# Kernel tuning notes

Hardware: AMD Instinct MI355X
Metric: run time of the kernel (lower is better)

Reference implementation:

```python
import jax, jax.numpy as jnp
import numpy as np

B, N, E = 4, 2048, 16384
ND, ED, TD, C, H = 256, 128, 64, 512, 8
DH = C // H
EPS = 1e-5


def setup_inputs() -> dict:
    key = jax.random.key(0)
    ks = jax.random.split(key, 28)
    w = lambda k, s: (jax.random.normal(k, s, jnp.float32) * 0.02)
    inp = {
        'x': jax.random.normal(ks[0], (B, N, ND), jnp.float32),
        'edge_attr': jax.random.normal(ks[1], (B, E, ED), jnp.float32),
        'timestamps': jax.random.uniform(ks[2], (B, N), jnp.float32),
        # FeatureProjection / TimeEncoder params (torch Linear layout: [out,in])
        'W_node': w(ks[3], (C, 2 * ND)), 'b_node': jnp.zeros((C,), jnp.float32),
        'W_temb': w(ks[4], (TD, 1)),     'b_temb': jnp.zeros((TD,), jnp.float32),
        'W_timef': w(ks[5], (C, 2 * TD)), 'b_timef': jnp.zeros((C,), jnp.float32),
        'W_edge': w(ks[6], (C, ED)),     'b_edge': jnp.zeros((C,), jnp.float32),
        # MultiheadAttention params
        'Wq': w(ks[7], (C, C)), 'bq': jnp.zeros((C,), jnp.float32),
        'Wk': w(ks[8], (C, C)), 'bk': jnp.zeros((C,), jnp.float32),
        'Wv': w(ks[9], (C, C)), 'bv': jnp.zeros((C,), jnp.float32),
        'Wo': w(ks[10], (C, C)), 'bo': jnp.zeros((C,), jnp.float32),
        # FFN
        'W1': w(ks[11], (4 * C, C)), 'b1': jnp.zeros((4 * C,), jnp.float32),
        'W2': w(ks[12], (C, 4 * C)), 'b2': jnp.zeros((C,), jnp.float32),
        # LayerNorms
        'g1': jnp.ones((C,), jnp.float32), 'be1': jnp.zeros((C,), jnp.float32),
        'g2': jnp.ones((C,), jnp.float32), 'be2': jnp.zeros((C,), jnp.float32),
        'edge_index': jax.random.randint(ks[13], (B, 2, E), 0, N, jnp.int64),
    }
    return inp


def _ln(x, g, b):
    m = jnp.mean(x, axis=-1, keepdims=True)
    v = jnp.mean((x - m) ** 2, axis=-1, keepdims=True)
    return (x - m) * jax.lax.rsqrt(v + EPS) * g + b


def reference(x, edge_attr, timestamps, W_node, b_node, W_temb, b_temb,
              W_timef, b_timef, W_edge, b_edge, Wq, bq, Wk, bk, Wv, bv,
              Wo, bo, W1, b1, W2, b2, g1, be1, g2, be2, edge_index):
    Bx, Nx, _ = x.shape
    # add self-loops
    loops = jnp.broadcast_to(jnp.arange(Nx, dtype=edge_index.dtype)[None, None, :], (Bx, 2, Nx))
    ei = jnp.concatenate([edge_index, loops], axis=2)          # [B,2,E+N]
    ea = jnp.concatenate([edge_attr, jnp.zeros((Bx, Nx, edge_attr.shape[-1]), edge_attr.dtype)], axis=1)
    src, tgt = ei[:, 0, :], ei[:, 1, :]                        # [B,Et]
    # batched gathers
    x_i = jnp.take_along_axis(x, src[:, :, None], axis=1)      # [B,Et,ND]
    x_j = jnp.take_along_axis(x, tgt[:, :, None], axis=1)
    t_i = jnp.take_along_axis(timestamps, src, axis=1)         # [B,Et]
    t_j = jnp.take_along_axis(timestamps, tgt, axis=1)
    # time encoder: sin(Linear(1->TD))
    t_i_enc = jnp.sin(t_i[..., None] * W_temb[:, 0] + b_temb)  # [B,Et,TD]
    t_j_enc = jnp.sin(t_j[..., None] * W_temb[:, 0] + b_temb)
    # projections (torch Linear: y = x @ W.T + b)
    node_f = jnp.concatenate([x_i, x_j], axis=-1) @ W_node.T + b_node        # [B,Et,C]
    time_f = jnp.concatenate([t_i_enc, t_j_enc], axis=-1) @ W_timef.T + b_timef
    edge_f = ea @ W_edge.T + b_edge
    # MultiheadAttention, batch_first=False: seq axis = dim0 (length B)
    L, Nb, _ = node_f.shape
    q = (node_f @ Wq.T + bq).reshape(L, Nb, H, DH)
    k = (time_f @ Wk.T + bk).reshape(L, Nb, H, DH)
    v = (edge_f @ Wv.T + bv).reshape(L, Nb, H, DH)
    scores = jnp.einsum('lnhd,mnhd->nhlm', q, k) / np.sqrt(DH)  # [Nb,H,L,L]
    attn = jax.nn.softmax(scores, axis=-1)
    ctx = jnp.einsum('nhlm,mnhd->lnhd', attn, v).reshape(L, Nb, C)
    attn_out = ctx @ Wo.T + bo
    out1 = _ln(node_f + attn_out, g1, be1)
    ffn = jax.nn.gelu(out1 @ W1.T + b1, approximate=False) @ W2.T + b2
    out2 = _ln(out1 + ffn, g2, be2)
    return out2
```

## Files before the change

### kernel.cpp

```cpp
#include <hip/hip_runtime.h>
#include <math.h>

#define BB 4
#define NN 2048
#define EE 16384
#define LL (EE + NN)
#define ND_ 256
#define ED_ 128
#define TD_ 64
#define CC 512
#define HH 8
#define DH_ 64
#define C4 2048

typedef unsigned short u16;
typedef unsigned int u32;
typedef __bf16 bhalf8 __attribute__((ext_vector_type(8)));
typedef float f32x4 __attribute__((ext_vector_type(4)));

struct GatherArgs {
    const float* x;
    const float* ts;
    const float* wtemb;
    const float* btemb;
    const float* eattr;
    const int*   ei;
};

__device__ __forceinline__ u16 f2bf(float f) {
    union { float f; unsigned u; } c; c.f = f;
    const unsigned r = (c.u + 0x7fffu + ((c.u >> 16) & 1u)) >> 16;
    return (u16)r;
}
__device__ __forceinline__ u16 f2bf_hw(float f) {
    __bf16 h = (__bf16)f;
    union { __bf16 h; u16 u; } c; c.h = h; return c.u;
}
__device__ __forceinline__ float bf2f(u16 u) {
    union { unsigned u; float f; } c; c.u = ((unsigned)u) << 16; return c.f;
}
__device__ __forceinline__ float gelu_fast(float v) {
    const float u = v * (0.7978845608f + 0.0356774081f * v * v);
    const float e = __expf(2.0f * u);
    const float t = 1.0f - 2.0f / (e + 1.0f);
    return 0.5f * v * (1.0f + t);
}

#define GLD16(gp, lp) __builtin_amdgcn_global_load_lds( \
    (const __attribute__((address_space(1))) unsigned int*)(gp), \
    (__attribute__((address_space(3))) unsigned int*)(lp), 16, 0, 0)

template<bool GELU>
__global__ __launch_bounds__(512, 2)
void gemm_mfma(const u16* __restrict__ A, const u16* __restrict__ W,
               const float* __restrict__ bias, u16* __restrict__ Y,
               int N, int K)
{
    __shared__ u16 As[2][16384];
    __shared__ u16 Bs[2][16384];

    const int o    = blockIdx.y * gridDim.x + blockIdx.x;
    const int nwg  = gridDim.x * gridDim.y;
    const int xcd  = o & 7;
    const int qq   = nwg >> 3, rr = nwg & 7;
    const int wg   = (xcd < rr ? xcd * (qq + 1) : rr * (qq + 1) + (xcd - rr) * qq) + (o >> 3);
    const int bx   = wg % gridDim.x;
    const int by   = wg / gridDim.x;
    const int m0   = by * 256;
    const int n0   = bx * 256;

    const int tid  = threadIdx.x;
    const int lane = tid & 63;
    const int wid  = tid >> 6;
    const int wm   = wid >> 2;
    const int wn   = wid & 3;

    const int swz8 = (((tid & 7) ^ ((tid >> 3) & 7))) * 8;
    const size_t sK = (size_t)K;
    const u16* Agb = A + (size_t)(m0 + (tid >> 3)) * sK + swz8;
    const u16* Wgb = W + (size_t)(n0 + (tid >> 3)) * sK + swz8;

    const int NT  = K >> 6;
    const int rlo = lane & 15;
    const int hi4 = lane >> 4;
    const int lk  = lane & 7;

#define STAGE_A(kt, h) do {                                      \
    const u16* _g = Agb + (size_t)(kt) * 64 + (size_t)(h) * 128 * sK; \
    u16* _l = &As[(kt) & 1][(h) * 8192 + tid * 8];               \
    GLD16(_g,           _l);                                     \
    GLD16(_g + 64 * sK, _l + 4096);                              \
} while (0)
#define STAGE_B(kt, h) do {                                      \
    const u16* _g = Wgb + (size_t)(kt) * 64 + (size_t)(h) * 128 * sK; \
    u16* _l = &Bs[(kt) & 1][(h) * 8192 + tid * 8];               \
    GLD16(_g,           _l);                                     \
    GLD16(_g + 64 * sK, _l + 4096);                              \
} while (0)

#define SWZOFF(ks) (((((ks) << 2) | hi4) ^ lk) << 3)
#define RD(buf, row, ks) (*(const bhalf8*)&(buf)[(row) * 64 + SWZOFF(ks)])

#define PHASE_SYNC() do {                                        \
    __builtin_amdgcn_sched_barrier(0);                           \
    __builtin_amdgcn_s_barrier();                                \
    asm volatile("s_waitcnt lgkmcnt(0)" ::: "memory");           \
    __builtin_amdgcn_sched_barrier(0);                           \
} while (0)
#define PHASE_END() do {                                         \
    __builtin_amdgcn_sched_barrier(0);                           \
    __builtin_amdgcn_s_barrier();                                \
    __builtin_amdgcn_sched_barrier(0);                           \
} while (0)

    f32x4 acc[8][4] = {};

    STAGE_A(0, 0); STAGE_A(0, 1);
    STAGE_B(0, 0); STAGE_B(0, 1);
    STAGE_B(1, 0); STAGE_B(1, 1);
    asm volatile("s_waitcnt vmcnt(4)" ::: "memory");
    __builtin_amdgcn_s_barrier();
    __builtin_amdgcn_sched_barrier(0);

    for (int t = 0; t < NT; ++t) {
        const u16* as = &As[t & 1][0];
        const u16* bs = &Bs[t & 1][0];
        bhalf8 aLo[4][2], aHi[4][2], b0[2][2], b1[2][2];

        #pragma unroll
        for (int i = 0; i < 4; ++i) {
            aLo[i][0] = RD(as, wm * 128 + i * 16 + rlo, 0);
            aLo[i][1] = RD(as, wm * 128 + i * 16 + rlo, 1);
        }
        #pragma unroll
        for (int j = 0; j < 2; ++j) {
            b0[j][0] = RD(bs, wn * 64 + j * 16 + rlo, 0);
            b0[j][1] = RD(bs, wn * 64 + j * 16 + rlo, 1);
        }
        if (t + 1 < NT) STAGE_A(t + 1, 0);
        PHASE_SYNC();
        __builtin_amdgcn_s_setprio(1);
        #pragma unroll
        for (int i = 0; i < 4; ++i)
            #pragma unroll
            for (int j = 0; j < 2; ++j)
                #pragma unroll
                for (int ks = 0; ks < 2; ++ks)
                    acc[i][j] = __builtin_amdgcn_mfma_f32_16x16x32_bf16(b0[j][ks], aLo[i][ks], acc[i][j], 0, 0, 0);
        __builtin_amdgcn_s_setprio(0);
        PHASE_END();

        #pragma unroll
        for (int j = 0; j < 2; ++j) {
            b1[j][0] = RD(bs, wn * 64 + 32 + j * 16 + rlo, 0);
            b1[j][1] = RD(bs, wn * 64 + 32 + j * 16 + rlo, 1);
        }
        if (t + 1 < NT) STAGE_A(t + 1, 1);
        PHASE_SYNC();
        __builtin_amdgcn_s_setprio(1);
        #pragma unroll
        for (int i = 0; i < 4; ++i)
            #pragma unroll
            for (int j = 0; j < 2; ++j)
                #pragma unroll
                for (int ks = 0; ks < 2; ++ks)
                    acc[i][2 + j] = __builtin_amdgcn_mfma_f32_16x16x32_bf16(b1[j][ks], aLo[i][ks], acc[i][2 + j], 0, 0, 0);
        __builtin_amdgcn_s_setprio(0);
        PHASE_END();

        #pragma unroll
        for (int i = 0; i < 4; ++i) {
            aHi[i][0] = RD(as, wm * 128 + 64 + i * 16 + rlo, 0);
            aHi[i][1] = RD(as, wm * 128 + 64 + i * 16 + rlo, 1);
        }
        if (t + 2 < NT) STAGE_B(t + 2, 0);
        PHASE_SYNC();
        __builtin_amdgcn_s_setprio(1);
        #pragma unroll
        for (int i = 0; i < 4; ++i)
            #pragma unroll
            for (int j = 0; j < 2; ++j)
                #pragma unroll
                for (int ks = 0; ks < 2; ++ks)
                    acc[4 + i][j] = __builtin_amdgcn_mfma_f32_16x16x32_bf16(b0[j][ks], aHi[i][ks], acc[4 + i][j], 0, 0, 0);
        __builtin_amdgcn_s_setprio(0);
        PHASE_END();

        if (t + 2 < NT) {
            STAGE_B(t + 2, 1);
            asm volatile("s_waitcnt vmcnt(4)" ::: "memory");
        } else if (t < NT - 1) {
            asm volatile("s_waitcnt vmcnt(0)" ::: "memory");
        }
        PHASE_SYNC();
        __builtin_amdgcn_s_setprio(1);
        #pragma unroll
        for (int i = 0; i < 4; ++i)
            #pragma unroll
            for (int j = 0; j < 2; ++j)
                #pragma unroll
                for (int ks = 0; ks < 2; ++ks)
                    acc[4 + i][2 + j] = __builtin_amdgcn_mfma_f32_16x16x32_bf16(b1[j][ks], aHi[i][ks], acc[4 + i][2 + j], 0, 0, 0);
        __builtin_amdgcn_s_setprio(0);
        if (t < NT - 1) PHASE_END();
    }
#undef STAGE_A
#undef STAGE_B
#undef SWZOFF
#undef RD
#undef PHASE_SYNC
#undef PHASE_END

    const int row0 = m0 + wm * 128;
    const int col0 = n0 + wn * 64;
    const int rq   = (lane >> 4) * 4;
    float4 bi[4];
    #pragma unroll
    for (int j = 0; j < 4; ++j)
        bi[j] = *(const float4*)(bias + col0 + j * 16 + rq);

    #pragma unroll
    for (int i = 0; i < 8; ++i) {
        const int gr = row0 + i * 16 + rlo;
        u16* yrow = Y + (size_t)gr * N + col0;
        #pragma unroll
        for (int j = 0; j < 4; ++j) {
            float v0 = acc[i][j][0] + bi[j].x;
            float v1 = acc[i][j][1] + bi[j].y;
            float v2 = acc[i][j][2] + bi[j].z;
            float v3 = acc[i][j][3] + bi[j].w;
            if constexpr (GELU) {
                v0 = gelu_fast(v0); v1 = gelu_fast(v1);
                v2 = gelu_fast(v2); v3 = gelu_fast(v3);
            }
            ushort4 ov;
            ov.x = f2bf_hw(v0); ov.y = f2bf_hw(v1);
            ov.z = f2bf_hw(v2); ov.w = f2bf_hw(v3);
            *(ushort4*)(yrow + j * 16 + rq) = ov;
        }
    }
}

__global__ __launch_bounds__(256)
void prep_kernel(u16* __restrict__ An, u16* __restrict__ Akv,
                 int e0, GatherArgs ga)
{
    const int r  = blockIdx.x;
    const int el = r >> 2;
    const int b  = r & 3;
    const int ge = e0 + el;
    const int t  = threadIdx.x;

    int isrc, itgt;
    if (ge < EE) {
        isrc = ga.ei[(b * 2 + 0) * EE + ge];
        itgt = ga.ei[(b * 2 + 1) * EE + ge];
    } else {
        isrc = itgt = ge - EE;
    }

    if (t < 128) {
        const int c = t * 4;
        const float* src = (c < ND_) ? (ga.x + ((size_t)b * NN + isrc) * ND_ + c)
                                     : (ga.x + ((size_t)b * NN + itgt) * ND_ + (c - ND_));
        const float4 vv = *(const float4*)src;
        ushort4 ov;
        ov.x = f2bf(vv.x); ov.y = f2bf(vv.y); ov.z = f2bf(vv.z); ov.w = f2bf(vv.w);
        *(ushort4*)(An + (size_t)r * 512 + c) = ov;
    } else if (t < 160) {
        const int c  = (t - 128) * 4;
        const float tt = (c < TD_) ? ga.ts[b * NN + isrc] : ga.ts[b * NN + itgt];
        const int  cb = (c < TD_) ? c : c - TD_;
        ushort4 ov;
        ov.x = f2bf(sinf(tt * ga.wtemb[cb + 0] + ga.btemb[cb + 0]));
        ov.y = f2bf(sinf(tt * ga.wtemb[cb + 1] + ga.btemb[cb + 1]));
        ov.z = f2bf(sinf(tt * ga.wtemb[cb + 2] + ga.btemb[cb + 2]));
        ov.w = f2bf(sinf(tt * ga.wtemb[cb + 3] + ga.btemb[cb + 3]));
        *(ushort4*)(Akv + (size_t)r * 256 + c) = ov;
    } else if (t < 192) {
        const int c = (t - 160) * 4;
        float4 vv = make_float4(0.f, 0.f, 0.f, 0.f);
        if (ge < EE) vv = *(const float4*)(ga.eattr + ((size_t)b * EE + ge) * ED_ + c);
        ushort4 ov;
        ov.x = f2bf(vv.x); ov.y = f2bf(vv.y); ov.z = f2bf(vv.z); ov.w = f2bf(vv.w);
        *(ushort4*)(Akv + (size_t)r * 256 + 128 + c) = ov;
    }
}

__global__ __launch_bounds__(256)
void comb_w_bf(const float* __restrict__ Wa, const float* __restrict__ Wb,
               u16* __restrict__ out, int Kin, int ostride)
{
    const int idx  = blockIdx.x * 256 + threadIdx.x;
    const int c    = idx / Kin;
    const int kcol = idx - c * Kin;
    float acc = 0.f;
    for (int j = 0; j < CC; j++)
        acc += Wa[c * CC + j] * Wb[j * Kin + kcol];
    out[(size_t)c * ostride + kcol] = f2bf(acc);
}

__global__ __launch_bounds__(256)
void comb_b(const float* __restrict__ Wa, const float* __restrict__ bin,
            const float* __restrict__ ba, float* __restrict__ bout)
{
    const int c = blockIdx.x * 256 + threadIdx.x;
    float acc = ba[c];
    for (int j = 0; j < CC; j++)
        acc += Wa[c * CC + j] * bin[j];
    bout[c] = acc;
}

__global__ __launch_bounds__(256)
void cvt_bf(const float* __restrict__ in, u16* __restrict__ out, int n)
{
    const int i = (blockIdx.x * 256 + threadIdx.x) * 4;
    if (i < n) {
        const float4 v = *(const float4*)(in + i);
        ushort4 ov;
        ov.x = f2bf(v.x); ov.y = f2bf(v.y); ov.z = f2bf(v.z); ov.w = f2bf(v.w);
        *(ushort4*)(out + i) = ov;
    }
}

__global__ __launch_bounds__(256)
void zero_u16(u16* __restrict__ p, int n)
{
    const int i = blockIdx.x * 256 + threadIdx.x;
    if (i < n) p[i] = 0;
}

__global__ __launch_bounds__(256)
void copy_f32(const float* __restrict__ in, float* __restrict__ out, int n)
{
    const int i = blockIdx.x * 256 + threadIdx.x;
    if (i < n) out[i] = in[i];
}

__global__ __launch_bounds__(256)
void attn_kernel(const u16* __restrict__ nodq, const u16* __restrict__ kv,
                 u16* __restrict__ ctx)
{
    const int e    = blockIdx.x * 4 + (threadIdx.x >> 6);
    const int lane = threadIdx.x & 63;
    const int off  = (lane >> 3) * 64 + (lane & 7) * 8;

    float qf[4][8], kf[4][8], vf[4][8];
    #pragma unroll
    for (int l = 0; l < 4; l++) {
        const size_t rq = (size_t)(4 * e + l) * 1024;
        const uint4 qv = *(const uint4*)(nodq + rq + 512 + off);
        const uint4 kx = *(const uint4*)(kv + rq + off);
        const uint4 vx = *(const uint4*)(kv + rq + 512 + off);
        const u32 qa[4] = {qv.x, qv.y, qv.z, qv.w};
        const u32 ka[4] = {kx.x, kx.y, kx.z, kx.w};
        const u32 va[4] = {vx.x, vx.y, vx.z, vx.w};
        #pragma unroll
        for (int p = 0; p < 4; p++) {
            qf[l][2*p] = bf2f((u16)qa[p]); qf[l][2*p+1] = bf2f((u16)(qa[p] >> 16));
            kf[l][2*p] = bf2f((u16)ka[p]); kf[l][2*p+1] = bf2f((u16)(ka[p] >> 16));
            vf[l][2*p] = bf2f((u16)va[p]); vf[l][2*p+1] = bf2f((u16)(va[p] >> 16));
        }
    }

    float sc[4][4];
    #pragma unroll
    for (int l = 0; l < 4; l++) {
        #pragma unroll
        for (int m = 0; m < 4; m++) {
            float p = 0.f;
            #pragma unroll
            for (int d = 0; d < 8; d++) p += qf[l][d] * kf[m][d];
            p += __shfl_xor(p, 1, 64);
            p += __shfl_xor(p, 2, 64);
            p += __shfl_xor(p, 4, 64);
            sc[l][m] = p * 0.125f;
        }
    }

    #pragma unroll
    for (int l = 0; l < 4; l++) {
        const float mx = fmaxf(fmaxf(sc[l][0], sc[l][1]), fmaxf(sc[l][2], sc[l][3]));
        float a[4], s = 0.f;
        #pragma unroll
        for (int m = 0; m < 4; m++) { a[m] = __expf(sc[l][m] - mx); s += a[m]; }
        const float inv = 1.0f / s;
        float cv[8];
        #pragma unroll
        for (int d = 0; d < 8; d++) {
            cv[d] = (a[0] * vf[0][d] + a[1] * vf[1][d] +
                     a[2] * vf[2][d] + a[3] * vf[3][d]) * inv;
        }
        ushort4 o0, o1;
        o0.x = f2bf(cv[0]); o0.y = f2bf(cv[1]); o0.z = f2bf(cv[2]); o0.w = f2bf(cv[3]);
        o1.x = f2bf(cv[4]); o1.y = f2bf(cv[5]); o1.z = f2bf(cv[6]); o1.w = f2bf(cv[7]);
        u16* crow = ctx + (size_t)(4 * e + l) * 512 + off;
        *(ushort4*)crow       = o0;
        *(ushort4*)(crow + 4) = o1;
    }
}

__global__ __launch_bounds__(256)
void ln1_kernel(const u16* __restrict__ nodq, const u16* __restrict__ aout,
                const float* __restrict__ g, const float* __restrict__ be,
                u16* __restrict__ outb)
{
    const int r    = blockIdx.x * 4 + (threadIdx.x >> 6);
    const int lane = threadIdx.x & 63;
    const int c    = lane * 8;

    const uint4 nf = *(const uint4*)(nodq + (size_t)r * 1024 + c);
    const uint4 ao = *(const uint4*)(aout + (size_t)r * 512 + c);
    const u32 na[4] = {nf.x, nf.y, nf.z, nf.w};
    const u32 aa[4] = {ao.x, ao.y, ao.z, ao.w};

    float v[8];
    #pragma unroll
    for (int p = 0; p < 4; p++) {
        v[2*p]   = bf2f((u16)na[p])         + bf2f((u16)aa[p]);
        v[2*p+1] = bf2f((u16)(na[p] >> 16)) + bf2f((u16)(aa[p] >> 16));
    }

    float s = 0.f;
    #pragma unroll
    for (int p = 0; p < 8; p++) s += v[p];
    #pragma unroll
    for (int o = 32; o; o >>= 1) s += __shfl_xor(s, o, 64);
    const float mean = s * (1.0f / 512.0f);

    float d[8], vs = 0.f;
    #pragma unroll
    for (int p = 0; p < 8; p++) { d[p] = v[p] - mean; vs += d[p] * d[p]; }
    #pragma unroll
    for (int o = 32; o; o >>= 1) vs += __shfl_xor(vs, o, 64);
    const float rstd = rsqrtf(vs * (1.0f / 512.0f) + 1e-5f);

    const float4 g0 = *(const float4*)(g + c),  g1 = *(const float4*)(g + c + 4);
    const float4 b0 = *(const float4*)(be + c), b1 = *(const float4*)(be + c + 4);
    const float gg[8] = {g0.x, g0.y, g0.z, g0.w, g1.x, g1.y, g1.z, g1.w};
    const float bb[8] = {b0.x, b0.y, b0.z, b0.w, b1.x, b1.y, b1.z, b1.w};

    uint4 ov;
    u32 w[4];
    #pragma unroll
    for (int p = 0; p < 4; p++) {
        const float y0 = d[2*p]   * rstd * gg[2*p]   + bb[2*p];
        const float y1 = d[2*p+1] * rstd * gg[2*p+1] + bb[2*p+1];
        w[p] = (u32)f2bf(y0) | ((u32)f2bf(y1) << 16);
    }
    ov.x = w[0]; ov.y = w[1]; ov.z = w[2]; ov.w = w[3];
    *(uint4*)(outb + (size_t)r * 512 + c) = ov;
}

__global__ __launch_bounds__(256)
void ln2_kernel(const u16* __restrict__ out1, const u16* __restrict__ ffn,
                const float* __restrict__ g, const float* __restrict__ be,
                float* __restrict__ out, int e0)
{
    const int r    = blockIdx.x * 4 + (threadIdx.x >> 6);
    const int lane = threadIdx.x & 63;
    const int c    = lane * 8;

    const uint4 o1 = *(const uint4*)(out1 + (size_t)r * 512 + c);
    const uint4 ff = *(const uint4*)(ffn  + (size_t)r * 512 + c);
    const u32 oa[4] = {o1.x, o1.y, o1.z, o1.w};
    const u32 fa[4] = {ff.x, ff.y, ff.z, ff.w};

    float v[8];
    #pragma unroll
    for (int p = 0; p < 4; p++) {
        v[2*p]   = bf2f((u16)oa[p])         + bf2f((u16)fa[p]);
        v[2*p+1] = bf2f((u16)(oa[p] >> 16)) + bf2f((u16)(fa[p] >> 16));
    }

    float s = 0.f;
    #pragma unroll
    for (int p = 0; p < 8; p++) s += v[p];
    #pragma unroll
    for (int o = 32; o; o >>= 1) s += __shfl_xor(s, o, 64);
    const float mean = s * (1.0f / 512.0f);

    float d[8], vs = 0.f;
    #pragma unroll
    for (int p = 0; p < 8; p++) { d[p] = v[p] - mean; vs += d[p] * d[p]; }
    #pragma unroll
    for (int o = 32; o; o >>= 1) vs += __shfl_xor(vs, o, 64);
    const float rstd = rsqrtf(vs * (1.0f / 512.0f) + 1e-5f);

    const float4 g0 = *(const float4*)(g + c),  g1 = *(const float4*)(g + c + 4);
    const float4 b0 = *(const float4*)(be + c), b1 = *(const float4*)(be + c + 4);

    const int el = r >> 2;
    const int b  = r & 3;
    float* orow = out + ((size_t)b * LL + e0 + el) * CC + c;
    float4 y0, y1;
    y0.x = d[0] * rstd * g0.x + b0.x;
    y0.y = d[1] * rstd * g0.y + b0.y;
    y0.z = d[2] * rstd * g0.z + b0.z;
    y0.w = d[3] * rstd * g0.w + b0.w;
    y1.x = d[4] * rstd * g1.x + b1.x;
    y1.y = d[5] * rstd * g1.y + b1.y;
    y1.z = d[6] * rstd * g1.z + b1.z;
    y1.w = d[7] * rstd * g1.w + b1.w;
    *(float4*)(orow)     = y0;
    *(float4*)(orow + 4) = y1;
}

extern "C" void kernel_launch(void* const* d_in, const int* in_sizes, int n_in,
                              void* d_out, int out_size, void* d_ws, size_t ws_size,
                              hipStream_t stream)
{
    const float* x       = (const float*)d_in[0];
    const float* eattr   = (const float*)d_in[1];
    const float* ts      = (const float*)d_in[2];
    const float* W_node  = (const float*)d_in[3];
    const float* b_node  = (const float*)d_in[4];
    const float* W_temb  = (const float*)d_in[5];
    const float* b_temb  = (const float*)d_in[6];
    const float* W_timef = (const float*)d_in[7];
    const float* b_timef = (const float*)d_in[8];
    const float* W_edge  = (const float*)d_in[9];
    const float* b_edge  = (const float*)d_in[10];
    const float* Wq      = (const float*)d_in[11];
    const float* bq      = (const float*)d_in[12];
    const float* Wk      = (const float*)d_in[13];
    const float* bk      = (const float*)d_in[14];
    const float* Wv      = (const float*)d_in[15];
    const float* bv      = (const float*)d_in[16];
    const float* Wo      = (const float*)d_in[17];
    const float* bo      = (const float*)d_in[18];
    const float* W1      = (const float*)d_in[19];
    const float* b1      = (const float*)d_in[20];
    const float* W2      = (const float*)d_in[21];
    const float* b2      = (const float*)d_in[22];
    const float* g1      = (const float*)d_in[23];
    const float* be1     = (const float*)d_in[24];
    const float* g2      = (const float*)d_in[25];
    const float* be2     = (const float*)d_in[26];
    const int*   ei      = (const int*)d_in[27];

    float* out = (float*)d_out;

    u16* wnq_cat = (u16*)d_ws;
    u16* wkv_cat = wnq_cat + 524288;
    u16* wo      = wkv_cat + 262144;
    u16* w1b     = wo + 262144;
    u16* w2b     = w1b + 1048576;
    float* bias_nq = (float*)(w2b + 1048576);
    float* bias_kv = bias_nq + 1024;
    char*  cbase   = (char*)(bias_kv + 1024);
    const size_t fixedB = (size_t)(cbase - (char*)d_ws);

    const size_t availB = (ws_size > fixedB) ? (ws_size - fixedB) : 0;
    int Ec = (int)(availB / 32768);
    Ec = (Ec / 64) * 64;
    if (Ec > LL) Ec = LL;
    if (Ec < 64) Ec = 64;

    const size_t rmax = (size_t)4 * Ec;
    u16* An   = (u16*)cbase;
    u16* nodq = An + rmax * 512;
    u16* R    = nodq + rmax * 1024;
    u16* Akv  = R;
    u16* kv   = R + rmax * 256;
    u16* hid  = R;
    u16* aout = R + rmax * 2048;

    GatherArgs ga{x, ts, W_temb, b_temb, eattr, ei};
    const dim3 blk(256);
    const dim3 gblk(512);

    cvt_bf   <<<dim3(256),  blk, 0, stream>>>(W_node, wnq_cat, 262144);
    comb_w_bf<<<dim3(1024), blk, 0, stream>>>(Wq, W_node, wnq_cat + 262144, 512, 512);
    zero_u16 <<<dim3(1024), blk, 0, stream>>>(wkv_cat, 262144);
    comb_w_bf<<<dim3(256),  blk, 0, stream>>>(Wk, W_timef, wkv_cat, 128, 256);
    comb_w_bf<<<dim3(256),  blk, 0, stream>>>(Wv, W_edge, wkv_cat + 512 * 256 + 128, 128, 256);
    cvt_bf   <<<dim3(256),  blk, 0, stream>>>(Wo, wo,  262144);
    cvt_bf   <<<dim3(1024), blk, 0, stream>>>(W1, w1b, 1048576);
    cvt_bf   <<<dim3(1024), blk, 0, stream>>>(W2, w2b, 1048576);
    copy_f32 <<<dim3(2),    blk, 0, stream>>>(b_node, bias_nq, 512);
    comb_b   <<<dim3(2),    blk, 0, stream>>>(Wq, b_node,  bq, bias_nq + 512);
    comb_b   <<<dim3(2),    blk, 0, stream>>>(Wk, b_timef, bk, bias_kv);
    comb_b   <<<dim3(2),    blk, 0, stream>>>(Wv, b_edge,  bv, bias_kv + 512);

    for (int e0 = 0; e0 < LL; e0 += Ec) {
        int ec = LL - e0; if (ec > Ec) ec = Ec;
        const int rows = 4 * ec;
        const int gy = rows / 256;

        prep_kernel<<<dim3(rows), blk, 0, stream>>>(An, Akv, e0, ga);

        gemm_mfma<false><<<dim3(4, gy), gblk, 0, stream>>>(An,  wnq_cat, bias_nq, nodq, 1024, 512);
        gemm_mfma<false><<<dim3(4, gy), gblk, 0, stream>>>(Akv, wkv_cat, bias_kv, kv,   1024, 256);

        attn_kernel<<<dim3(ec / 4), blk, 0, stream>>>(nodq, kv, An );

        gemm_mfma<false><<<dim3(2, gy), gblk, 0, stream>>>(An, wo, bo, aout, 512, 512);
        ln1_kernel<<<dim3(rows / 4), blk, 0, stream>>>(nodq, aout, g1, be1, An );

        gemm_mfma<true ><<<dim3(8, gy), gblk, 0, stream>>>(An,  w1b, b1, hid, 2048, 512);
        gemm_mfma<false><<<dim3(2, gy), gblk, 0, stream>>>(hid, w2b, b2, aout , 512, 2048);

        ln2_kernel<<<dim3(rows / 4), blk, 0, stream>>>(An, aout, g2, be2, out, e0);
    }
}
```

Baseline: 1.329 ms.

## Precompute per-node projections and gather them per edge instead of per-edge GEMMs

The node and time projections are linear in the gathered source and target features, so they are now computed once per node (2048 per batch) and stored in tables P and KLR. The attention and first layernorm kernels then gather and add the source and target halves by edge index, so the large per-edge node and query projection GEMM and the time/key GEMM no longer run. Only the edge-value GEMM stays per edge. The cost is extra fixed workspace and random gathers of 2048-wide rows, plus bf16 rounding that now happens per half before the sum.

New measurement: 1.135 ms (median of 2 runs). -14.6%, faster.

```diff
diff --git a/kernel.cpp b/kernel.cpp
--- a/kernel.cpp
+++ b/kernel.cpp
@@ -17,15 +17,6 @@
 typedef unsigned int u32;
 typedef __bf16 bhalf8 __attribute__((ext_vector_type(8)));
 typedef float f32x4 __attribute__((ext_vector_type(4)));
-
-struct GatherArgs {
-    const float* x;
-    const float* ts;
-    const float* wtemb;
-    const float* btemb;
-    const float* eattr;
-    const int*   ei;
-};
 
 __device__ __forceinline__ u16 f2bf(float f) {
     union { float f; unsigned u; } c; c.f = f;
@@ -242,49 +233,90 @@
 }
 
 __global__ __launch_bounds__(256)
-void prep_kernel(u16* __restrict__ An, u16* __restrict__ Akv,
-                 int e0, GatherArgs ga)
-{
-    const int r  = blockIdx.x;
+void build_wbig(const float* __restrict__ Wn, const float* __restrict__ Wq,
+                u16* __restrict__ out)
+{
+    const int idx = blockIdx.x * 256 + threadIdx.x;
+    const int R = idx >> 8;
+    const int k = idx & 255;
+    float v;
+    if (R < 512) {
+        v = Wn[R * 512 + k];
+    } else if (R < 1024) {
+        const int c = R - 512; float a = 0.f;
+        for (int j = 0; j < 512; j++) a += Wq[c * 512 + j] * Wn[j * 512 + k];
+        v = a;
+    } else if (R < 1536) {
+        v = Wn[(R - 1024) * 512 + 256 + k];
+    } else {
+        const int c = R - 1536; float a = 0.f;
+        for (int j = 0; j < 512; j++) a += Wq[c * 512 + j] * Wn[j * 512 + 256 + k];
+        v = a;
+    }
+    out[idx] = f2bf(v);
+}
+
+__global__ __launch_bounds__(256)
+void build_wkt(const float* __restrict__ Wk, const float* __restrict__ Wtf,
+               u16* __restrict__ out)
+{
+    const int idx = blockIdx.x * 256 + threadIdx.x;
+    const int R = idx >> 8;
+    const int k = idx & 255;
+    float v = 0.f;
+    const bool live = (k < 128) && ((R < 512) ? (k < 64) : (k >= 64));
+    if (live) {
+        const int c = (R < 512) ? R : R - 512;
+        float a = 0.f;
+        for (int j = 0; j < 512; j++) a += Wk[c * 512 + j] * Wtf[j * 128 + k];
+        v = a;
+    }
+    out[idx] = f2bf(v);
+}
+
+__global__ __launch_bounds__(256)
+void te_kernel(const float* __restrict__ ts, const float* __restrict__ wtemb,
+               const float* __restrict__ btemb, u16* __restrict__ TE)
+{
+    const int idx4 = (blockIdx.x * 256 + threadIdx.x) * 4;
+    const int n = idx4 >> 8;
+    const int j = idx4 & 255;
+    ushort4 ov;
+    if (j < 128) {
+        const int kb = j & 63;
+        const float tt = ts[n];
+        ov.x = f2bf(sinf(tt * wtemb[kb + 0] + btemb[kb + 0]));
+        ov.y = f2bf(sinf(tt * wtemb[kb + 1] + btemb[kb + 1]));
+        ov.z = f2bf(sinf(tt * wtemb[kb + 2] + btemb[kb + 2]));
+        ov.w = f2bf(sinf(tt * wtemb[kb + 3] + btemb[kb + 3]));
+    } else {
+        ov.x = ov.y = ov.z = ov.w = 0;
+    }
+    *(ushort4*)(TE + idx4) = ov;
+}
+
+__global__ __launch_bounds__(256)
+void prep_e(const float* __restrict__ eattr, u16* __restrict__ Ae, int e0)
+{
+    const int t  = threadIdx.x;
+    const int r  = blockIdx.x * 8 + (t >> 5);
+    const int cl = (t & 31) * 8;
     const int el = r >> 2;
     const int b  = r & 3;
     const int ge = e0 + el;
-    const int t  = threadIdx.x;
-
-    int isrc, itgt;
-    if (ge < EE) {
-        isrc = ga.ei[(b * 2 + 0) * EE + ge];
-        itgt = ga.ei[(b * 2 + 1) * EE + ge];
+    uint4 ov;
+    if (ge < EE && cl < 128) {
+        const float* src = eattr + ((size_t)b * EE + ge) * 128 + cl;
+        const float4 a = *(const float4*)src;
+        const float4 c = *(const float4*)(src + 4);
+        ov.x = (u32)f2bf(a.x) | ((u32)f2bf(a.y) << 16);
+        ov.y = (u32)f2bf(a.z) | ((u32)f2bf(a.w) << 16);
+        ov.z = (u32)f2bf(c.x) | ((u32)f2bf(c.y) << 16);
+        ov.w = (u32)f2bf(c.z) | ((u32)f2bf(c.w) << 16);
     } else {
-        isrc = itgt = ge - EE;
-    }
-
-    if (t < 128) {
-        const int c = t * 4;
-        const float* src = (c < ND_) ? (ga.x + ((size_t)b * NN + isrc) * ND_ + c)
-                                     : (ga.x + ((size_t)b * NN + itgt) * ND_ + (c - ND_));
-        const float4 vv = *(const float4*)src;
-        ushort4 ov;
-        ov.x = f2bf(vv.x); ov.y = f2bf(vv.y); ov.z = f2bf(vv.z); ov.w = f2bf(vv.w);
-        *(ushort4*)(An + (size_t)r * 512 + c) = ov;
-    } else if (t < 160) {
-        const int c  = (t - 128) * 4;
-        const float tt = (c < TD_) ? ga.ts[b * NN + isrc] : ga.ts[b * NN + itgt];
-        const int  cb = (c < TD_) ? c : c - TD_;
-        ushort4 ov;
-        ov.x = f2bf(sinf(tt * ga.wtemb[cb + 0] + ga.btemb[cb + 0]));
-        ov.y = f2bf(sinf(tt * ga.wtemb[cb + 1] + ga.btemb[cb + 1]));
-        ov.z = f2bf(sinf(tt * ga.wtemb[cb + 2] + ga.btemb[cb + 2]));
-        ov.w = f2bf(sinf(tt * ga.wtemb[cb + 3] + ga.btemb[cb + 3]));
-        *(ushort4*)(Akv + (size_t)r * 256 + c) = ov;
-    } else if (t < 192) {
-        const int c = (t - 160) * 4;
-        float4 vv = make_float4(0.f, 0.f, 0.f, 0.f);
-        if (ge < EE) vv = *(const float4*)(ga.eattr + ((size_t)b * EE + ge) * ED_ + c);
-        ushort4 ov;
-        ov.x = f2bf(vv.x); ov.y = f2bf(vv.y); ov.z = f2bf(vv.z); ov.w = f2bf(vv.w);
-        *(ushort4*)(Akv + (size_t)r * 256 + 128 + c) = ov;
-    }
+        ov.x = ov.y = ov.z = ov.w = 0;
+    }
+    *(uint4*)(Ae + (size_t)r * 256 + cl) = ov;
 }
 
 __global__ __launch_bounds__(256)
@@ -338,28 +370,45 @@
 }
 
 __global__ __launch_bounds__(256)
-void attn_kernel(const u16* __restrict__ nodq, const u16* __restrict__ kv,
-                 u16* __restrict__ ctx)
-{
-    const int e    = blockIdx.x * 4 + (threadIdx.x >> 6);
+void attn_fused(const u16* __restrict__ P, const u16* __restrict__ KLR,
+                const u16* __restrict__ kvv, const int* __restrict__ ei,
+                u16* __restrict__ ctx, int e0)
+{
+    const int el   = blockIdx.x * 4 + (threadIdx.x >> 6);
+    const int ge   = e0 + el;
     const int lane = threadIdx.x & 63;
     const int off  = (lane >> 3) * 64 + (lane & 7) * 8;
 
     float qf[4][8], kf[4][8], vf[4][8];
     #pragma unroll
     for (int l = 0; l < 4; l++) {
-        const size_t rq = (size_t)(4 * e + l) * 1024;
-        const uint4 qv = *(const uint4*)(nodq + rq + 512 + off);
-        const uint4 kx = *(const uint4*)(kv + rq + off);
-        const uint4 vx = *(const uint4*)(kv + rq + 512 + off);
-        const u32 qa[4] = {qv.x, qv.y, qv.z, qv.w};
-        const u32 ka[4] = {kx.x, kx.y, kx.z, kx.w};
+        int s, t;
+        if (ge < EE) {
+            s = ei[(l * 2 + 0) * EE + ge];
+            t = ei[(l * 2 + 1) * EE + ge];
+        } else {
+            s = t = ge - EE;
+        }
+        const size_t ns = (size_t)(l * NN + s);
+        const size_t nt = (size_t)(l * NN + t);
+        const uint4 qs = *(const uint4*)(P + ns * 2048 + 512 + off);
+        const uint4 qt = *(const uint4*)(P + nt * 2048 + 1536 + off);
+        const uint4 ks = *(const uint4*)(KLR + ns * 1024 + off);
+        const uint4 kt = *(const uint4*)(KLR + nt * 1024 + 512 + off);
+        const uint4 vx = *(const uint4*)(kvv + (size_t)(4 * el + l) * 512 + off);
+        const u32 qa[4] = {qs.x, qs.y, qs.z, qs.w};
+        const u32 qb[4] = {qt.x, qt.y, qt.z, qt.w};
+        const u32 ka[4] = {ks.x, ks.y, ks.z, ks.w};
+        const u32 kb[4] = {kt.x, kt.y, kt.z, kt.w};
         const u32 va[4] = {vx.x, vx.y, vx.z, vx.w};
         #pragma unroll
         for (int p = 0; p < 4; p++) {
-            qf[l][2*p] = bf2f((u16)qa[p]); qf[l][2*p+1] = bf2f((u16)(qa[p] >> 16));
-            kf[l][2*p] = bf2f((u16)ka[p]); kf[l][2*p+1] = bf2f((u16)(ka[p] >> 16));
-            vf[l][2*p] = bf2f((u16)va[p]); vf[l][2*p+1] = bf2f((u16)(va[p] >> 16));
+            qf[l][2*p]   = bf2f((u16)qa[p])         + bf2f((u16)qb[p]);
+            qf[l][2*p+1] = bf2f((u16)(qa[p] >> 16)) + bf2f((u16)(qb[p] >> 16));
+            kf[l][2*p]   = bf2f((u16)ka[p])         + bf2f((u16)kb[p]);
+            kf[l][2*p+1] = bf2f((u16)(ka[p] >> 16)) + bf2f((u16)(kb[p] >> 16));
+            vf[l][2*p]   = bf2f((u16)va[p]);
+            vf[l][2*p+1] = bf2f((u16)(va[p] >> 16));
         }
     }
 
@@ -394,39 +443,53 @@
         ushort4 o0, o1;
         o0.x = f2bf(cv[0]); o0.y = f2bf(cv[1]); o0.z = f2bf(cv[2]); o0.w = f2bf(cv[3]);
         o1.x = f2bf(cv[4]); o1.y = f2bf(cv[5]); o1.z = f2bf(cv[6]); o1.w = f2bf(cv[7]);
-        u16* crow = ctx + (size_t)(4 * e + l) * 512 + off;
+        u16* crow = ctx + (size_t)(4 * el + l) * 512 + off;
         *(ushort4*)crow       = o0;
         *(ushort4*)(crow + 4) = o1;
     }
 }
 
 __global__ __launch_bounds__(256)
-void ln1_kernel(const u16* __restrict__ nodq, const u16* __restrict__ aout,
-                const float* __restrict__ g, const float* __restrict__ be,
-                u16* __restrict__ outb)
+void ln1_fused(const u16* __restrict__ P, const u16* __restrict__ aout,
+               const int* __restrict__ ei,
+               const float* __restrict__ g, const float* __restrict__ be,
+               u16* __restrict__ outb, int e0)
 {
     const int r    = blockIdx.x * 4 + (threadIdx.x >> 6);
     const int lane = threadIdx.x & 63;
     const int c    = lane * 8;
-
-    const uint4 nf = *(const uint4*)(nodq + (size_t)r * 1024 + c);
-    const uint4 ao = *(const uint4*)(aout + (size_t)r * 512 + c);
-    const u32 na[4] = {nf.x, nf.y, nf.z, nf.w};
+    const int el   = r >> 2;
+    const int b    = r & 3;
+    const int ge   = e0 + el;
+
+    int s, t;
+    if (ge < EE) {
+        s = ei[(b * 2 + 0) * EE + ge];
+        t = ei[(b * 2 + 1) * EE + ge];
+    } else {
+        s = t = ge - EE;
+    }
+
+    const uint4 nfs = *(const uint4*)(P + (size_t)(b * NN + s) * 2048 + c);
+    const uint4 nft = *(const uint4*)(P + (size_t)(b * NN + t) * 2048 + 1024 + c);
+    const uint4 ao  = *(const uint4*)(aout + (size_t)r * 512 + c);
+    const u32 na[4] = {nfs.x, nfs.y, nfs.z, nfs.w};
+    const u32 nb[4] = {nft.x, nft.y, nft.z, nft.w};
     const u32 aa[4] = {ao.x, ao.y, ao.z, ao.w};
 
     float v[8];
     #pragma unroll
     for (int p = 0; p < 4; p++) {
-        v[2*p]   = bf2f((u16)na[p])         + bf2f((u16)aa[p]);
-        v[2*p+1] = bf2f((u16)(na[p] >> 16)) + bf2f((u16)(aa[p] >> 16));
-    }
-
-    float s = 0.f;
-    #pragma unroll
-    for (int p = 0; p < 8; p++) s += v[p];
-    #pragma unroll
-    for (int o = 32; o; o >>= 1) s += __shfl_xor(s, o, 64);
-    const float mean = s * (1.0f / 512.0f);
+        v[2*p]   = bf2f((u16)na[p])         + bf2f((u16)nb[p])         + bf2f((u16)aa[p]);
+        v[2*p+1] = bf2f((u16)(na[p] >> 16)) + bf2f((u16)(nb[p] >> 16)) + bf2f((u16)(aa[p] >> 16));
+    }
+
+    float sum = 0.f;
+    #pragma unroll
+    for (int p = 0; p < 8; p++) sum += v[p];
+    #pragma unroll
+    for (int o = 32; o; o >>= 1) sum += __shfl_xor(sum, o, 64);
+    const float mean = sum * (1.0f / 512.0f);
 
     float d[8], vs = 0.f;
     #pragma unroll
@@ -541,65 +604,74 @@
 
     float* out = (float*)d_out;
 
-    u16* wnq_cat = (u16*)d_ws;
-    u16* wkv_cat = wnq_cat + 524288;
-    u16* wo      = wkv_cat + 262144;
-    u16* w1b     = wo + 262144;
-    u16* w2b     = w1b + 1048576;
-    float* bias_nq = (float*)(w2b + 1048576);
-    float* bias_kv = bias_nq + 1024;
-    char*  cbase   = (char*)(bias_kv + 1024);
+    u16* wbig = (u16*)d_ws;
+    u16* wkt  = wbig + 524288;
+    u16* wev  = wkt + 262144;
+    u16* wo   = wev + 131072;
+    u16* w1b  = wo + 262144;
+    u16* w2b  = w1b + 1048576;
+    u16* xb   = w2b + 1048576;
+    u16* TE   = xb + 2097152;
+    u16* P    = TE + 2097152;
+    u16* KLR  = P + 16777216;
+    float* bias2048 = (float*)(KLR + 8388608);
+    float* biasKLR  = bias2048 + 2048;
+    float* bev      = biasKLR + 1024;
+    char*  cbase    = (char*)(bev + 512);
     const size_t fixedB = (size_t)(cbase - (char*)d_ws);
 
     const size_t availB = (ws_size > fixedB) ? (ws_size - fixedB) : 0;
-    int Ec = (int)(availB / 32768);
+    int Ec = (int)(availB / 30720);
     Ec = (Ec / 64) * 64;
     if (Ec > LL) Ec = LL;
     if (Ec < 64) Ec = 64;
 
     const size_t rmax = (size_t)4 * Ec;
-    u16* An   = (u16*)cbase;
-    u16* nodq = An + rmax * 512;
-    u16* R    = nodq + rmax * 1024;
-    u16* Akv  = R;
-    u16* kv   = R + rmax * 256;
-    u16* hid  = R;
-    u16* aout = R + rmax * 2048;
-
-    GatherArgs ga{x, ts, W_temb, b_temb, eattr, ei};
+    u16* Ae   = (u16*)cbase;
+    u16* kvv  = Ae + rmax * 256;
+    u16* An   = kvv + rmax * 512;
+    u16* aout = An + rmax * 512;
+    u16* hid  = aout + rmax * 512;
+
     const dim3 blk(256);
     const dim3 gblk(512);
 
-    cvt_bf   <<<dim3(256),  blk, 0, stream>>>(W_node, wnq_cat, 262144);
-    comb_w_bf<<<dim3(1024), blk, 0, stream>>>(Wq, W_node, wnq_cat + 262144, 512, 512);
-    zero_u16 <<<dim3(1024), blk, 0, stream>>>(wkv_cat, 262144);
-    comb_w_bf<<<dim3(256),  blk, 0, stream>>>(Wk, W_timef, wkv_cat, 128, 256);
-    comb_w_bf<<<dim3(256),  blk, 0, stream>>>(Wv, W_edge, wkv_cat + 512 * 256 + 128, 128, 256);
-    cvt_bf   <<<dim3(256),  blk, 0, stream>>>(Wo, wo,  262144);
-    cvt_bf   <<<dim3(1024), blk, 0, stream>>>(W1, w1b, 1048576);
-    cvt_bf   <<<dim3(1024), blk, 0, stream>>>(W2, w2b, 1048576);
-    copy_f32 <<<dim3(2),    blk, 0, stream>>>(b_node, bias_nq, 512);
-    comb_b   <<<dim3(2),    blk, 0, stream>>>(Wq, b_node,  bq, bias_nq + 512);
-    comb_b   <<<dim3(2),    blk, 0, stream>>>(Wk, b_timef, bk, bias_kv);
-    comb_b   <<<dim3(2),    blk, 0, stream>>>(Wv, b_edge,  bv, bias_kv + 512);
+    cvt_bf    <<<dim3(2048), blk, 0, stream>>>(x, xb, 2097152);
+    build_wbig<<<dim3(2048), blk, 0, stream>>>(W_node, Wq, wbig);
+    copy_f32  <<<dim3(2),    blk, 0, stream>>>(b_node, bias2048, 512);
+    comb_b    <<<dim3(2),    blk, 0, stream>>>(Wq, b_node, bq, bias2048 + 512);
+    zero_u16  <<<dim3(8),    blk, 0, stream>>>((u16*)(bias2048 + 1024), 2048);
+    gemm_mfma<false><<<dim3(8, 32), gblk, 0, stream>>>(xb, wbig, bias2048, P, 2048, 256);
+
+    te_kernel <<<dim3(2048), blk, 0, stream>>>(ts, W_temb, b_temb, TE);
+    build_wkt <<<dim3(1024), blk, 0, stream>>>(Wk, W_timef, wkt);
+    comb_b    <<<dim3(2),    blk, 0, stream>>>(Wk, b_timef, bk, biasKLR);
+    zero_u16  <<<dim3(4),    blk, 0, stream>>>((u16*)(biasKLR + 512), 1024);
+    gemm_mfma<false><<<dim3(4, 32), gblk, 0, stream>>>(TE, wkt, biasKLR, KLR, 1024, 256);
+
+    zero_u16  <<<dim3(512),  blk, 0, stream>>>(wev, 131072);
+    comb_w_bf <<<dim3(256),  blk, 0, stream>>>(Wv, W_edge, wev, 128, 256);
+    comb_b    <<<dim3(2),    blk, 0, stream>>>(Wv, b_edge, bv, bev);
+    cvt_bf    <<<dim3(256),  blk, 0, stream>>>(Wo, wo,  262144);
+    cvt_bf    <<<dim3(1024), blk, 0, stream>>>(W1, w1b, 1048576);
+    cvt_bf    <<<dim3(1024), blk, 0, stream>>>(W2, w2b, 1048576);
 
     for (int e0 = 0; e0 < LL; e0 += Ec) {
         int ec = LL - e0; if (ec > Ec) ec = Ec;
         const int rows = 4 * ec;
         const int gy = rows / 256;
 
-        prep_kernel<<<dim3(rows), blk, 0, stream>>>(An, Akv, e0, ga);
-
-        gemm_mfma<false><<<dim3(4, gy), gblk, 0, stream>>>(An,  wnq_cat, bias_nq, nodq, 1024, 512);
-        gemm_mfma<false><<<dim3(4, gy), gblk, 0, stream>>>(Akv, wkv_cat, bias_kv, kv,   1024, 256);
-
-        attn_kernel<<<dim3(ec / 4), blk, 0, stream>>>(nodq, kv, An );
+        prep_e<<<dim3(rows / 8), blk, 0, stream>>>(eattr, Ae, e0);
+
+        gemm_mfma<false><<<dim3(2, gy), gblk, 0, stream>>>(Ae, wev, bev, kvv, 512, 256);
+
+        attn_fused<<<dim3(ec / 4), blk, 0, stream>>>(P, KLR, kvv, ei, An, e0);
 
         gemm_mfma<false><<<dim3(2, gy), gblk, 0, stream>>>(An, wo, bo, aout, 512, 512);
-        ln1_kernel<<<dim3(rows / 4), blk, 0, stream>>>(nodq, aout, g1, be1, An );
+        ln1_fused<<<dim3(rows / 4), blk, 0, stream>>>(P, aout, ei, g1, be1, An, e0);
 
         gemm_mfma<true ><<<dim3(8, gy), gblk, 0, stream>>>(An,  w1b, b1, hid, 2048, 512);
-        gemm_mfma<false><<<dim3(2, gy), gblk, 0, stream>>>(hid, w2b, b2, aout , 512, 2048);
+        gemm_mfma<false><<<dim3(2, gy), gblk, 0, stream>>>(hid, w2b, b2, aout, 512, 2048);
 
         ln2_kernel<<<dim3(rows / 4), blk, 0, stream>>>(An, aout, g2, be2, out, e0);
     }
```
